# Kernel tuning notes

Hardware: AMD Instinct MI355X
Metric: run time of the kernel (lower is better)

Reference implementation:

```python
import jax, jax.numpy as jnp
import numpy as np

N_V = 6890  # SMPL vertices
N_J = 24    # SMPL joints
# standard SMPL kinematic tree: PARENT[i-1] is parent of joint i (i=1..23)
PARENT = np.array([0, 0, 0, 1, 2, 3, 4, 5, 6, 7, 8, 9, 9, 9, 12, 13, 14, 16, 17, 18, 19, 20, 21], dtype=np.int64)


def rodrigues(r):
    """Axis-angle [N,3] -> rotation matrices [N,3,3] (batch Rodrigues)."""
    angle = jnp.sqrt(jnp.sum(r * r, axis=-1, keepdims=True) + 1e-8)  # [N,1]
    axis = r / angle
    c = jnp.cos(angle)[..., None]  # [N,1,1]
    s = jnp.sin(angle)[..., None]
    x, y, z = axis[..., 0], axis[..., 1], axis[..., 2]
    zeros = jnp.zeros_like(x)
    K = jnp.stack([zeros, -z, y, z, zeros, -x, -y, x, zeros], axis=-1).reshape(-1, 3, 3)
    outer = axis[..., :, None] * axis[..., None, :]
    I = jnp.eye(3, dtype=r.dtype)
    return c * I + (1.0 - c) * outer + s * K


def setup_inputs() -> dict:
    key = jax.random.key(0)
    ks = jax.random.split(key, 7)
    B = 1024
    pose = jax.random.normal(ks[0], (B, 72), dtype=jnp.float32) * 0.4
    beta = jax.random.normal(ks[1], (B, 10), dtype=jnp.float32)
    shapedirs = jax.random.normal(ks[2], (N_V, 3, 10), dtype=jnp.float32) * 0.03
    posedirs = jax.random.normal(ks[3], (N_V, 3, 207), dtype=jnp.float32) * 0.01
    v_template = jax.random.normal(ks[4], (N_V, 3), dtype=jnp.float32)
    Jreg = jax.random.uniform(ks[5], (N_J, N_V), dtype=jnp.float32)
    J_regressor = Jreg / jnp.sum(Jreg, axis=1, keepdims=True)  # rows sum to 1 like SMPL
    w = jax.random.uniform(ks[6], (N_V, N_J), dtype=jnp.float32)
    weights = w / jnp.sum(w, axis=1, keepdims=True)  # convex skinning weights
    return {"pose": pose, "beta": beta, "shapedirs": shapedirs, "posedirs": posedirs,
            "v_template": v_template, "J_regressor": J_regressor, "weights": weights}


def reference(pose, beta, shapedirs, posedirs, v_template, J_regressor, weights):
    B = pose.shape[0]
    # shape blend shapes: v_shaped = shapedirs @ beta + template  [B,6890,3]
    v_shaped = jnp.einsum('vcs,bs->bvc', shapedirs, beta) + v_template[None]
    J = jnp.einsum('jv,bvc->bjc', J_regressor, v_shaped)
    # pose -> rotation matrices
    R = rodrigues(pose.reshape(-1, 3)).reshape(B, N_J, 3, 3)
    # pose blend shapes from (R - I) of non-root joints  [B,207]
    lrotmin = (R[:, 1:] - jnp.eye(3, dtype=R.dtype)).reshape(B, 207)
    v_posed = v_shaped + jnp.einsum('vcp,bp->bvc', posedirs, lrotmin)
    # relative joint locations
    J_rel = jnp.concatenate([J[:, :1], J[:, 1:] - J[:, PARENT]], axis=1)  # [B,24,3]
    # local transforms [B,24,4,4]
    G_top = jnp.concatenate([R, J_rel[..., None]], axis=-1)  # [B,24,3,4]
    pad_row = jnp.broadcast_to(jnp.array([0., 0., 0., 1.], dtype=R.dtype), (B, N_J, 1, 4))
    G_local = jnp.concatenate([G_top, pad_row], axis=2)
    # forward kinematics along the chain (fixed 24-joint loop)
    Gs = [G_local[:, 0]]
    for i in range(1, N_J):
        Gs.append(jnp.matmul(Gs[PARENT[i - 1]], G_local[:, i]))
    G = jnp.stack(Gs, axis=1)  # [B,24,4,4]
    # remove rest-pose transform: subtract G @ [J,0] from last column
    J_h = jnp.concatenate([J, jnp.zeros((B, N_J, 1), dtype=J.dtype)], axis=2)  # [B,24,4]
    corr = jnp.einsum('bjmn,bjn->bjm', G, J_h)  # [B,24,4]
    G = G - jnp.pad(corr[..., None], ((0, 0), (0, 0), (0, 0), (3, 0)))
    # skinning: per-vertex transform T = weights @ G  [B,6890,4,4]
    T = jnp.einsum('vj,bjmn->bvmn', weights, G)
    v_h = jnp.concatenate([v_posed, jnp.ones((B, N_V, 1), dtype=v_posed.dtype)], axis=-1)
    v = jnp.einsum('bvmn,bvn->bvm', T, v_h)[..., :3]
    return v
```

## Files before the change

### kernel.cpp

```cpp
#include <hip/hip_runtime.h>
#include <hip/hip_bf16.h>

#define N_V 6890
#define NVPAD 6912
#define N_J 24
#define NREAL 20670
#define NPROWS 27648
#define KDIM 224
#define FB 64
#define FV 64
#define SHP 260
#define NXT 108

typedef __attribute__((ext_vector_type(8))) short bf16x8;
typedef __attribute__((ext_vector_type(4))) float f32x4;

__constant__ int c_par[23] = {0,0,0,1,2,3,4,5,6,7,8,9,9,9,12,13,14,16,17,18,19,20,21};

static __device__ __forceinline__ unsigned short f2bf(float f) {
    unsigned int u = __float_as_uint(f);
    unsigned int r = (u + 0x7fffu + ((u >> 16) & 1u)) >> 16;
    return (unsigned short)r;
}
static __device__ __forceinline__ unsigned int pkbf(float a, float b) {
    return ((__float_as_uint(a) + 0x8000u) >> 16) |
           ((__float_as_uint(b) + 0x8000u) & 0xffff0000u);
}
static __device__ __forceinline__ size_t fragidx(int r, int k) {
    return ((size_t)((r >> 4) * 7 + (k >> 5)) << 9) +
           ((size_t)((r & 15) + (((k >> 3) & 3) << 4)) << 3) + (k & 7);
}

#define WS_PARTIAL 0
#define WS_USHORT  7128
#define U_AMF  0
#define U_BPF  229376
#define U_GBF  6422528
#define U_WBF  6946816

#define JREG_BLOCKS 192
#define BPF_BLOCKS  (NPROWS / 16)
#define WBF_BLOCKS  (NVPAD * 32 / 256)

static __device__ __forceinline__ float bval(const float* pd, const float* sd,
                                             const float* vt, int nc, int k) {
    if (k < 207)  return pd[(size_t)nc * 207 + k];
    if (k < 217)  return sd[(size_t)nc * 10 + (k - 207)];
    if (k == 217) return vt[nc];
    return 0.f;
}

__global__ __launch_bounds__(256)
void k_pre(const float* __restrict__ Jreg,
           const float* __restrict__ shapedirs,
           const float* __restrict__ v_template,
           const float* __restrict__ posedirs,
           const float* __restrict__ weights,
           float* __restrict__ partial,
           unsigned short* __restrict__ Bpf,
           unsigned short* __restrict__ Wbf) {
    const int bid = blockIdx.x;
    const int tid = threadIdx.x;

    if (bid < JREG_BLOCKS) {
        const int j = bid >> 3, chunk = bid & 7;
        const int per = (N_V + 7) / 8;
        const int v0 = chunk * per;
        const int v1 = (v0 + per < N_V) ? (v0 + per) : N_V;
        float acc[33];
#pragma unroll
        for (int k = 0; k < 33; ++k) acc[k] = 0.f;
        for (int v = v0 + tid; v < v1; v += 256) {
            const float w = Jreg[j * N_V + v];
            const float* sd = shapedirs + (size_t)v * 30;
#pragma unroll
            for (int k = 0; k < 30; ++k) acc[k] += w * sd[k];
            acc[30] += w * v_template[v * 3 + 0];
            acc[31] += w * v_template[v * 3 + 1];
            acc[32] += w * v_template[v * 3 + 2];
        }
#pragma unroll
        for (int k = 0; k < 33; ++k) {
            float x = acc[k];
            for (int off = 32; off > 0; off >>= 1) x += __shfl_down(x, off);
            acc[k] = x;
        }
        __shared__ float red[4][33];
        const int wave = tid >> 6, lane = tid & 63;
        if (lane == 0) {
#pragma unroll
            for (int k = 0; k < 33; ++k) red[wave][k] = acc[k];
        }
        __syncthreads();
        if (tid < 33) {
            partial[(j * 8 + chunk) * 33 + tid] =
                red[0][tid] + red[1][tid] + red[2][tid] + red[3][tid];
        }
    } else if (bid < JREG_BLOCKS + BPF_BLOCKS) {
        __shared__ float tile[16][228];
        const int r16 = bid - JREG_BLOCKS;
        for (int idx = tid; idx < 16 * 224; idx += 256) {
            const int row = idx / 224;
            const int k = idx - row * 224;
            const int np = r16 * 16 + row;
            const int v = np >> 2, cc = np & 3;
            float val = 0.f;
            if (cc < 3 && v < N_V) val = bval(posedirs, shapedirs, v_template, v * 3 + cc, k);
            tile[row][k] = val;
        }
        __syncthreads();
        const int l = tid >> 2;
        const int row = l & 15;
        const int kblk = (l >> 4) * 8;
        const int e2 = (tid & 3) * 2;
        unsigned short* dst = Bpf + ((size_t)r16 * 7) * 512 + (size_t)tid * 2;
#pragma unroll
        for (int ks = 0; ks < 7; ++ks) {
            const int k = ks * 32 + kblk + e2;
            ushort2 o;
            o.x = f2bf(tile[row][k]);
            o.y = f2bf(tile[row][k + 1]);
            *(ushort2*)(dst + (size_t)ks * 512) = o;
        }
    } else {
        const int idx = (bid - JREG_BLOCKS - BPF_BLOCKS) * 256 + tid;
        const int v = idx >> 5, k = idx & 31;
        float val = (v < N_V && k < 24) ? weights[(size_t)v * 24 + k] : 0.f;
        Wbf[idx] = f2bf(val);
    }
}

__global__ __launch_bounds__(64)
void k_joints(const float* __restrict__ pose, const float* __restrict__ beta,
              const float* __restrict__ partial,
              unsigned short* __restrict__ Amf,
              unsigned short* __restrict__ Gbf) {
    const int b = blockIdx.x;
    const int j = threadIdx.x;
    __shared__ float sJS[24][30];
    __shared__ float sJt[24][3];
    __shared__ float sJ[24][3];
    __shared__ float sG[24][12];

    for (int idx = j; idx < 792; idx += 64) {
        const int jj = idx / 33, kk = idx - jj * 33;
        float s = 0.f;
#pragma unroll
        for (int c = 0; c < 8; ++c) s += partial[(jj * 8 + c) * 33 + kk];
        if (kk < 30) sJS[jj][kk] = s;
        else         sJt[jj][kk - 30] = s;
    }

    for (int idx = j; idx < 224; idx += 64) {
        int mn, jj;
        if (idx < 128) { mn = 12 + (idx >> 5); jj = idx & 31; }
        else { const int q = idx - 128; mn = q >> 3; jj = 24 + (q & 7); }
        Gbf[(size_t)b * 512 + mn * 32 + jj] = 0;
    }
    __syncthreads();

    float R[9];
    if (j < 24) {
        const float* bt = beta + b * 10;
#pragma unroll
        for (int c = 0; c < 3; ++c) {
            float s = sJt[j][c];
#pragma unroll
            for (int t = 0; t < 10; ++t) s += sJS[j][c * 10 + t] * bt[t];
            sJ[j][c] = s;
        }
        const float rx = pose[b * 72 + 3 * j + 0];
        const float ry = pose[b * 72 + 3 * j + 1];
        const float rz = pose[b * 72 + 3 * j + 2];
        const float ang = sqrtf(rx * rx + ry * ry + rz * rz + 1e-8f);
        const float inv = 1.f / ang;
        const float x = rx * inv, y = ry * inv, z = rz * inv;
        const float c = cosf(ang), s = sinf(ang);
        const float ic = 1.f - c;
        R[0] = c + ic * x * x;     R[1] = ic * x * y - s * z; R[2] = ic * x * z + s * y;
        R[3] = ic * x * y + s * z; R[4] = c + ic * y * y;     R[5] = ic * y * z - s * x;
        R[6] = ic * x * z - s * y; R[7] = ic * y * z + s * x; R[8] = c + ic * z * z;
        if (j >= 1) {
            const int kb = (j - 1) * 9;
#pragma unroll
            for (int k = 0; k < 9; ++k)
                Amf[fragidx(b & 15, kb + k) + (size_t)(b >> 4) * 3584] =
                    f2bf(R[k] - ((k == 0 || k == 4 || k == 8) ? 1.f : 0.f));
        }
    } else if (j < 41) {
        const int k = 207 + (j - 24);
        float val = (k < 217) ? beta[b * 10 + (k - 207)] : (k == 217 ? 1.f : 0.f);
        Amf[fragidx(b & 15, k) + (size_t)(b >> 4) * 3584] = f2bf(val);
    }
    __syncthreads();
    if (j < 24) {
        float t0, t1, t2;
        if (j == 0) { t0 = sJ[0][0]; t1 = sJ[0][1]; t2 = sJ[0][2]; }
        else {
            const int p = c_par[j - 1];
            t0 = sJ[j][0] - sJ[p][0]; t1 = sJ[j][1] - sJ[p][1]; t2 = sJ[j][2] - sJ[p][2];
        }
        sG[j][0] = R[0]; sG[j][1] = R[1]; sG[j][2]  = R[2]; sG[j][3]  = t0;
        sG[j][4] = R[3]; sG[j][5] = R[4]; sG[j][6]  = R[5]; sG[j][7]  = t1;
        sG[j][8] = R[6]; sG[j][9] = R[7]; sG[j][10] = R[8]; sG[j][11] = t2;
    }
    __syncthreads();
    if (j == 0) {
        for (int i = 1; i < 24; ++i) {
            const int p = c_par[i - 1];
            float P[12], L[12];
#pragma unroll
            for (int k = 0; k < 12; ++k) { P[k] = sG[p][k]; L[k] = sG[i][k]; }
#pragma unroll
            for (int m = 0; m < 3; ++m) {
#pragma unroll
                for (int n = 0; n < 3; ++n)
                    sG[i][m * 4 + n] = P[m * 4] * L[n] + P[m * 4 + 1] * L[4 + n] + P[m * 4 + 2] * L[8 + n];
                sG[i][m * 4 + 3] = P[m * 4] * L[3] + P[m * 4 + 1] * L[7] + P[m * 4 + 2] * L[11] + P[m * 4 + 3];
            }
        }
    }
    __syncthreads();
    if (j < 24) {
        const float jx = sJ[j][0], jy = sJ[j][1], jz = sJ[j][2];
#pragma unroll
        for (int m = 0; m < 3; ++m) {
            const float corr = sG[j][m * 4] * jx + sG[j][m * 4 + 1] * jy + sG[j][m * 4 + 2] * jz;
            Gbf[(size_t)b * 512 + (m * 4 + 0) * 32 + j] = f2bf(sG[j][m * 4 + 0]);
            Gbf[(size_t)b * 512 + (m * 4 + 1) * 32 + j] = f2bf(sG[j][m * 4 + 1]);
            Gbf[(size_t)b * 512 + (m * 4 + 2) * 32 + j] = f2bf(sG[j][m * 4 + 2]);
            Gbf[(size_t)b * 512 + (m * 4 + 3) * 32 + j] = f2bf(sG[j][m * 4 + 3] - corr);
        }
    }
}

__global__ __launch_bounds__(256, 2)
void k_fused(const unsigned short* __restrict__ Amf,
             const unsigned short* __restrict__ Bpf,
             const unsigned short* __restrict__ Gbf,
             const unsigned short* __restrict__ Wbf,
             float* __restrict__ out) {
    __shared__ unsigned short sH[FB * SHP];
    const int tid = threadIdx.x;
    const int wid = tid >> 6, l = tid & 63;
    const int c16 = l & 15, p = l >> 4;

    const int wg = ((blockIdx.x & 7) * 216) + (blockIdx.x >> 3);
    const int xt = wg >> 4;
    const int bg = wg & 15;
    const int v0 = xt * FV;
    const int b0 = bg * FB;

    bf16x8 bw[4];
#pragma unroll
    for (int g = 0; g < 4; ++g)
        bw[g] = *(const bf16x8*)&Wbf[(size_t)(v0 + g * 16 + c16) * 32 + p * 8];
    const int bwv = wid * 16;
    const unsigned short* gG = Gbf + (size_t)(b0 + bwv) * 512 + c16 * 32 + p * 8;

    f32x4 acc[4][4];
#pragma unroll
    for (int i = 0; i < 4; ++i)
#pragma unroll
        for (int j = 0; j < 4; ++j) acc[i][j] = (f32x4){0.f, 0.f, 0.f, 0.f};

    const unsigned short* pbf = Bpf + ((size_t)(xt * 16 + wid * 4) * 7) * 512 + (size_t)l * 8;
    const unsigned short* pam = Amf + ((size_t)(bg * 4) * 7) * 512 + (size_t)l * 8;

#pragma unroll
    for (int ks = 0; ks < 7; ++ks) {
        bf16x8 af[4], bfr[4];
#pragma unroll
        for (int mi = 0; mi < 4; ++mi)
            af[mi] = *(const bf16x8*)(pbf + (size_t)(mi * 7 + ks) * 512);
#pragma unroll
        for (int bj = 0; bj < 4; ++bj)
            bfr[bj] = *(const bf16x8*)(pam + (size_t)(bj * 7 + ks) * 512);
#pragma unroll
        for (int mi = 0; mi < 4; ++mi)
#pragma unroll
            for (int bj = 0; bj < 4; ++bj)
                acc[mi][bj] = __builtin_amdgcn_mfma_f32_16x16x32_bf16(af[mi], bfr[bj], acc[mi][bj], 0, 0, 0);
    }

    bf16x8 agA[8], agB[8];
#pragma unroll
    for (int j = 0; j < 8; ++j)
        agA[j] = *(const bf16x8*)(gG + (size_t)j * 512);

    {
        const int vbase = wid * 16 + p;
#pragma unroll
        for (int mi = 0; mi < 4; ++mi) {
#pragma unroll
            for (int bj = 0; bj < 4; ++bj) {
                const int vl = vbase + mi * 4;
                const int bl = bj * 16 + c16;
                uint2 u;
                u.x = pkbf(acc[mi][bj][0], acc[mi][bj][1]);
                u.y = pkbf(acc[mi][bj][2], acc[mi][bj][3]);
                *(uint2*)&sH[bl * SHP + vl * 4] = u;
            }
        }
    }
    __syncthreads();

#pragma unroll
    for (int j = 0; j < 8; ++j)
        agB[j] = *(const bf16x8*)(gG + (size_t)(8 + j) * 512);

    bool st[4];
    float* o[4];
#pragma unroll
    for (int g = 0; g < 4; ++g) {
        st[g] = (v0 + g * 16 + c16 < N_V) && (p < 3);
        o[g] = out + (size_t)(b0 + bwv) * NREAL + (size_t)(v0 + g * 16 + c16) * 3 + p;
    }
    const unsigned short* sh = &sH[bwv * SHP + c16 * 4];

#pragma unroll
    for (int j = 0; j < 8; ++j) {
#pragma unroll
        for (int g = 0; g < 4; ++g) {
            const f32x4 t = __builtin_amdgcn_mfma_f32_16x16x32_bf16(agA[j], bw[g], (f32x4){0.f,0.f,0.f,0.f}, 0, 0, 0);
            const uint2 h = *(const uint2*)(sh + j * SHP + g * 64);
            const float x = __uint_as_float(h.x << 16);
            const float y = __uint_as_float(h.x & 0xffff0000u);
            const float z = __uint_as_float(h.y << 16);
            const float r = t[0] * x + t[1] * y + t[2] * z + t[3];
            if (st[g]) o[g][(size_t)j * NREAL] = r;
        }
    }
#pragma unroll
    for (int j = 0; j < 8; ++j) {
#pragma unroll
        for (int g = 0; g < 4; ++g) {
            const f32x4 t = __builtin_amdgcn_mfma_f32_16x16x32_bf16(agB[j], bw[g], (f32x4){0.f,0.f,0.f,0.f}, 0, 0, 0);
            const uint2 h = *(const uint2*)(sh + (8 + j) * SHP + g * 64);
            const float x = __uint_as_float(h.x << 16);
            const float y = __uint_as_float(h.x & 0xffff0000u);
            const float z = __uint_as_float(h.y << 16);
            const float r = t[0] * x + t[1] * y + t[2] * z + t[3];
            if (st[g]) o[g][(size_t)(8 + j) * NREAL] = r;
        }
    }
}

extern "C" void kernel_launch(void* const* d_in, const int* in_sizes, int n_in,
                              void* d_out, int out_size, void* d_ws, size_t ws_size,
                              hipStream_t stream) {
    const float* pose       = (const float*)d_in[0];
    const float* beta       = (const float*)d_in[1];
    const float* shapedirs  = (const float*)d_in[2];
    const float* posedirs   = (const float*)d_in[3];
    const float* v_template = (const float*)d_in[4];
    const float* Jreg       = (const float*)d_in[5];
    const float* weights    = (const float*)d_in[6];
    float* out = (float*)d_out;

    const int B = in_sizes[0] / 72;

    float* ws = (float*)d_ws;
    float* partial = ws + WS_PARTIAL;
    unsigned short* ubase = (unsigned short*)(ws + WS_USHORT);
    unsigned short* Amf = ubase + U_AMF;
    unsigned short* Bpf = ubase + U_BPF;
    unsigned short* Gbf = ubase + U_GBF;
    unsigned short* Wbf = ubase + U_WBF;

    k_pre<<<JREG_BLOCKS + BPF_BLOCKS + WBF_BLOCKS, 256, 0, stream>>>(
        Jreg, shapedirs, v_template, posedirs, weights, partial, Bpf, Wbf);
    k_joints<<<B, 64, 0, stream>>>(pose, beta, partial, Amf, Gbf);
    k_fused<<<NXT * (B / FB), 256, 0, stream>>>(Amf, Bpf, Gbf, Wbf, out);
}
```

Measured before the change: 80.96 us.

## Split fused kernel work over eight waves and batch four samples per joints block

The fused blend/skinning kernel now runs 512 threads per block, so each wave handles 8 batch rows and 2 vertex m-tiles instead of 16 and 4. This halves per-wave accumulator and G-fragment registers so more waves can be resident, at the cost of more blocks reloading shared operands. The joints kernel now processes four batch samples per 256-thread block, which amortises the reduction of the shared regressor partials across samples. Output addressing is simplified to a single base pointer plus offsets.

```diff
diff --git a/kernel.cpp b/kernel.cpp
--- a/kernel.cpp
+++ b/kernel.cpp
@@ -130,25 +130,27 @@
     }
 }
 
-__global__ __launch_bounds__(64)
+__global__ __launch_bounds__(256)
 void k_joints(const float* __restrict__ pose, const float* __restrict__ beta,
               const float* __restrict__ partial,
               unsigned short* __restrict__ Amf,
               unsigned short* __restrict__ Gbf) {
-    const int b = blockIdx.x;
-    const int j = threadIdx.x;
+    const int tid = threadIdx.x;
+    const int wid = tid >> 6;
+    const int j = tid & 63;
+    const int b = blockIdx.x * 4 + wid;
     __shared__ float sJS[24][30];
-    __shared__ float sJt[24][3];
-    __shared__ float sJ[24][3];
-    __shared__ float sG[24][12];
-
-    for (int idx = j; idx < 792; idx += 64) {
+    __shared__ float sJt_[24][3];
+    __shared__ float sJ[4][24][3];
+    __shared__ float sG[4][24][12];
+
+    for (int idx = tid; idx < 792; idx += 256) {
         const int jj = idx / 33, kk = idx - jj * 33;
         float s = 0.f;
 #pragma unroll
         for (int c = 0; c < 8; ++c) s += partial[(jj * 8 + c) * 33 + kk];
         if (kk < 30) sJS[jj][kk] = s;
-        else         sJt[jj][kk - 30] = s;
+        else         sJt_[jj][kk - 30] = s;
     }
 
     for (int idx = j; idx < 224; idx += 64) {
@@ -164,10 +166,10 @@
         const float* bt = beta + b * 10;
 #pragma unroll
         for (int c = 0; c < 3; ++c) {
-            float s = sJt[j][c];
+            float s = sJt_[j][c];
 #pragma unroll
             for (int t = 0; t < 10; ++t) s += sJS[j][c * 10 + t] * bt[t];
-            sJ[j][c] = s;
+            sJ[wid][j][c] = s;
         }
         const float rx = pose[b * 72 + 3 * j + 0];
         const float ry = pose[b * 72 + 3 * j + 1];
@@ -195,14 +197,16 @@
     __syncthreads();
     if (j < 24) {
         float t0, t1, t2;
-        if (j == 0) { t0 = sJ[0][0]; t1 = sJ[0][1]; t2 = sJ[0][2]; }
+        if (j == 0) { t0 = sJ[wid][0][0]; t1 = sJ[wid][0][1]; t2 = sJ[wid][0][2]; }
         else {
             const int p = c_par[j - 1];
-            t0 = sJ[j][0] - sJ[p][0]; t1 = sJ[j][1] - sJ[p][1]; t2 = sJ[j][2] - sJ[p][2];
-        }
-        sG[j][0] = R[0]; sG[j][1] = R[1]; sG[j][2]  = R[2]; sG[j][3]  = t0;
-        sG[j][4] = R[3]; sG[j][5] = R[4]; sG[j][6]  = R[5]; sG[j][7]  = t1;
-        sG[j][8] = R[6]; sG[j][9] = R[7]; sG[j][10] = R[8]; sG[j][11] = t2;
+            t0 = sJ[wid][j][0] - sJ[wid][p][0];
+            t1 = sJ[wid][j][1] - sJ[wid][p][1];
+            t2 = sJ[wid][j][2] - sJ[wid][p][2];
+        }
+        sG[wid][j][0] = R[0]; sG[wid][j][1] = R[1]; sG[wid][j][2]  = R[2]; sG[wid][j][3]  = t0;
+        sG[wid][j][4] = R[3]; sG[wid][j][5] = R[4]; sG[wid][j][6]  = R[5]; sG[wid][j][7]  = t1;
+        sG[wid][j][8] = R[6]; sG[wid][j][9] = R[7]; sG[wid][j][10] = R[8]; sG[wid][j][11] = t2;
     }
     __syncthreads();
     if (j == 0) {
@@ -210,31 +214,31 @@
             const int p = c_par[i - 1];
             float P[12], L[12];
 #pragma unroll
-            for (int k = 0; k < 12; ++k) { P[k] = sG[p][k]; L[k] = sG[i][k]; }
+            for (int k = 0; k < 12; ++k) { P[k] = sG[wid][p][k]; L[k] = sG[wid][i][k]; }
 #pragma unroll
             for (int m = 0; m < 3; ++m) {
 #pragma unroll
                 for (int n = 0; n < 3; ++n)
-                    sG[i][m * 4 + n] = P[m * 4] * L[n] + P[m * 4 + 1] * L[4 + n] + P[m * 4 + 2] * L[8 + n];
-                sG[i][m * 4 + 3] = P[m * 4] * L[3] + P[m * 4 + 1] * L[7] + P[m * 4 + 2] * L[11] + P[m * 4 + 3];
+                    sG[wid][i][m * 4 + n] = P[m * 4] * L[n] + P[m * 4 + 1] * L[4 + n] + P[m * 4 + 2] * L[8 + n];
+                sG[wid][i][m * 4 + 3] = P[m * 4] * L[3] + P[m * 4 + 1] * L[7] + P[m * 4 + 2] * L[11] + P[m * 4 + 3];
             }
         }
     }
     __syncthreads();
     if (j < 24) {
-        const float jx = sJ[j][0], jy = sJ[j][1], jz = sJ[j][2];
+        const float jx = sJ[wid][j][0], jy = sJ[wid][j][1], jz = sJ[wid][j][2];
 #pragma unroll
         for (int m = 0; m < 3; ++m) {
-            const float corr = sG[j][m * 4] * jx + sG[j][m * 4 + 1] * jy + sG[j][m * 4 + 2] * jz;
-            Gbf[(size_t)b * 512 + (m * 4 + 0) * 32 + j] = f2bf(sG[j][m * 4 + 0]);
-            Gbf[(size_t)b * 512 + (m * 4 + 1) * 32 + j] = f2bf(sG[j][m * 4 + 1]);
-            Gbf[(size_t)b * 512 + (m * 4 + 2) * 32 + j] = f2bf(sG[j][m * 4 + 2]);
-            Gbf[(size_t)b * 512 + (m * 4 + 3) * 32 + j] = f2bf(sG[j][m * 4 + 3] - corr);
-        }
-    }
-}
-
-__global__ __launch_bounds__(256, 2)
+            const float corr = sG[wid][j][m * 4] * jx + sG[wid][j][m * 4 + 1] * jy + sG[wid][j][m * 4 + 2] * jz;
+            Gbf[(size_t)b * 512 + (m * 4 + 0) * 32 + j] = f2bf(sG[wid][j][m * 4 + 0]);
+            Gbf[(size_t)b * 512 + (m * 4 + 1) * 32 + j] = f2bf(sG[wid][j][m * 4 + 1]);
+            Gbf[(size_t)b * 512 + (m * 4 + 2) * 32 + j] = f2bf(sG[wid][j][m * 4 + 2]);
+            Gbf[(size_t)b * 512 + (m * 4 + 3) * 32 + j] = f2bf(sG[wid][j][m * 4 + 3] - corr);
+        }
+    }
+}
+
+__global__ __launch_bounds__(512, 4)
 void k_fused(const unsigned short* __restrict__ Amf,
              const unsigned short* __restrict__ Bpf,
              const unsigned short* __restrict__ Gbf,
@@ -255,43 +259,43 @@
 #pragma unroll
     for (int g = 0; g < 4; ++g)
         bw[g] = *(const bf16x8*)&Wbf[(size_t)(v0 + g * 16 + c16) * 32 + p * 8];
-    const int bwv = wid * 16;
+    const int bwv = wid * 8;
     const unsigned short* gG = Gbf + (size_t)(b0 + bwv) * 512 + c16 * 32 + p * 8;
 
-    f32x4 acc[4][4];
-#pragma unroll
-    for (int i = 0; i < 4; ++i)
+    f32x4 acc[2][4];
+#pragma unroll
+    for (int i = 0; i < 2; ++i)
 #pragma unroll
         for (int j = 0; j < 4; ++j) acc[i][j] = (f32x4){0.f, 0.f, 0.f, 0.f};
 
-    const unsigned short* pbf = Bpf + ((size_t)(xt * 16 + wid * 4) * 7) * 512 + (size_t)l * 8;
+    const unsigned short* pbf = Bpf + ((size_t)(xt * 16 + wid * 2) * 7) * 512 + (size_t)l * 8;
     const unsigned short* pam = Amf + ((size_t)(bg * 4) * 7) * 512 + (size_t)l * 8;
 
 #pragma unroll
     for (int ks = 0; ks < 7; ++ks) {
-        bf16x8 af[4], bfr[4];
-#pragma unroll
-        for (int mi = 0; mi < 4; ++mi)
+        bf16x8 af[2], bfr[4];
+#pragma unroll
+        for (int mi = 0; mi < 2; ++mi)
             af[mi] = *(const bf16x8*)(pbf + (size_t)(mi * 7 + ks) * 512);
 #pragma unroll
         for (int bj = 0; bj < 4; ++bj)
             bfr[bj] = *(const bf16x8*)(pam + (size_t)(bj * 7 + ks) * 512);
 #pragma unroll
-        for (int mi = 0; mi < 4; ++mi)
+        for (int mi = 0; mi < 2; ++mi)
 #pragma unroll
             for (int bj = 0; bj < 4; ++bj)
                 acc[mi][bj] = __builtin_amdgcn_mfma_f32_16x16x32_bf16(af[mi], bfr[bj], acc[mi][bj], 0, 0, 0);
     }
 
-    bf16x8 agA[8], agB[8];
-#pragma unroll
-    for (int j = 0; j < 8; ++j)
+    bf16x8 agA[4], agB[4];
+#pragma unroll
+    for (int j = 0; j < 4; ++j)
         agA[j] = *(const bf16x8*)(gG + (size_t)j * 512);
 
     {
-        const int vbase = wid * 16 + p;
-#pragma unroll
-        for (int mi = 0; mi < 4; ++mi) {
+        const int vbase = wid * 8 + p;
+#pragma unroll
+        for (int mi = 0; mi < 2; ++mi) {
 #pragma unroll
             for (int bj = 0; bj < 4; ++bj) {
                 const int vl = vbase + mi * 4;
@@ -306,20 +310,18 @@
     __syncthreads();
 
 #pragma unroll
-    for (int j = 0; j < 8; ++j)
-        agB[j] = *(const bf16x8*)(gG + (size_t)(8 + j) * 512);
+    for (int j = 0; j < 4; ++j)
+        agB[j] = *(const bf16x8*)(gG + (size_t)(4 + j) * 512);
 
     bool st[4];
-    float* o[4];
-#pragma unroll
-    for (int g = 0; g < 4; ++g) {
+#pragma unroll
+    for (int g = 0; g < 4; ++g)
         st[g] = (v0 + g * 16 + c16 < N_V) && (p < 3);
-        o[g] = out + (size_t)(b0 + bwv) * NREAL + (size_t)(v0 + g * 16 + c16) * 3 + p;
-    }
+    float* ob = out + (size_t)(b0 + bwv) * NREAL + (size_t)(v0 + c16) * 3 + p;
     const unsigned short* sh = &sH[bwv * SHP + c16 * 4];
 
 #pragma unroll
-    for (int j = 0; j < 8; ++j) {
+    for (int j = 0; j < 4; ++j) {
 #pragma unroll
         for (int g = 0; g < 4; ++g) {
             const f32x4 t = __builtin_amdgcn_mfma_f32_16x16x32_bf16(agA[j], bw[g], (f32x4){0.f,0.f,0.f,0.f}, 0, 0, 0);
@@ -328,20 +330,20 @@
             const float y = __uint_as_float(h.x & 0xffff0000u);
             const float z = __uint_as_float(h.y << 16);
             const float r = t[0] * x + t[1] * y + t[2] * z + t[3];
-            if (st[g]) o[g][(size_t)j * NREAL] = r;
-        }
-    }
-#pragma unroll
-    for (int j = 0; j < 8; ++j) {
+            if (st[g]) ob[(size_t)j * NREAL + g * 48] = r;
+        }
+    }
+#pragma unroll
+    for (int j = 0; j < 4; ++j) {
 #pragma unroll
         for (int g = 0; g < 4; ++g) {
             const f32x4 t = __builtin_amdgcn_mfma_f32_16x16x32_bf16(agB[j], bw[g], (f32x4){0.f,0.f,0.f,0.f}, 0, 0, 0);
-            const uint2 h = *(const uint2*)(sh + (8 + j) * SHP + g * 64);
+            const uint2 h = *(const uint2*)(sh + (4 + j) * SHP + g * 64);
             const float x = __uint_as_float(h.x << 16);
             const float y = __uint_as_float(h.x & 0xffff0000u);
             const float z = __uint_as_float(h.y << 16);
             const float r = t[0] * x + t[1] * y + t[2] * z + t[3];
-            if (st[g]) o[g][(size_t)(8 + j) * NREAL] = r;
+            if (st[g]) ob[(size_t)(4 + j) * NREAL + g * 48] = r;
         }
     }
 }
@@ -370,6 +372,6 @@
 
     k_pre<<<JREG_BLOCKS + BPF_BLOCKS + WBF_BLOCKS, 256, 0, stream>>>(
         Jreg, shapedirs, v_template, posedirs, weights, partial, Bpf, Wbf);
-    k_joints<<<B, 64, 0, stream>>>(pose, beta, partial, Amf, Gbf);
-    k_fused<<<NXT * (B / FB), 256, 0, stream>>>(Amf, Bpf, Gbf, Wbf, out);
-}
+    k_joints<<<B / 4, 256, 0, stream>>>(pose, beta, partial, Amf, Gbf);
+    k_fused<<<NXT * (B / FB), 512, 0, stream>>>(Amf, Bpf, Gbf, Wbf, out);
+}
```

After: 74.43 us. 1.09x faster.
